# Optimization experiments

Hardware: AMD Instinct MI355X
Metric: run time of the kernel (lower is better)

Reference implementation:

```python
import jax, jax.numpy as jnp
import numpy as np

B, T, F, E, H = 1024, 128, 32, 16, 20
EPS = 1e-3  # keras BatchNormalization default epsilon
D = T * F   # flatten dim; fc1 builds with units = T*F due to pre-build units mutation


def lstm_relu(x, Wk, Wr, b, return_seq):
    """Keras LSTM with activation='relu', recurrent_activation=sigmoid.
    Gate order i, f, c(g), o. x: [B,T,Fin]. Returns [B,T,H] or [B,H]."""
    Bn = x.shape[0]
    h0 = jnp.zeros((Bn, H), x.dtype)
    c0 = jnp.zeros((Bn, H), x.dtype)

    def step(carry, xt):
        h, c = carry
        z = xt @ Wk + h @ Wr + b                      # [B, 4H]
        i, f, g, o = jnp.split(z, 4, axis=-1)
        i = jax.nn.sigmoid(i)
        f = jax.nn.sigmoid(f)
        g = jax.nn.relu(g)
        o = jax.nn.sigmoid(o)
        c = f * c + i * g
        h = o * jax.nn.relu(c)
        return (h, c), h

    (hT, _), hs = jax.lax.scan(step, (h0, c0), jnp.swapaxes(x, 0, 1))
    return jnp.swapaxes(hs, 0, 1) if return_seq else hT


def setup_inputs():
    key = jax.random.key(0)
    ks = jax.random.split(key, 16)
    s = 0.1
    d = {}
    d["x"] = jax.random.normal(ks[0], (B, T, F), jnp.float32)
    # BatchNorm (inference: moving stats)
    d["bn_gamma"] = jnp.ones((F,), jnp.float32)
    d["bn_beta"] = jnp.zeros((F,), jnp.float32)
    d["bn_mean"] = jax.random.normal(ks[1], (F,), jnp.float32) * 0.1
    d["bn_var"] = jax.random.uniform(ks[2], (F,), jnp.float32, 0.5, 1.5)
    # Per-expert LSTM stacks (stacked over expert axis E)
    d["k1"] = jax.random.normal(ks[3], (E, F, 4 * H), jnp.float32) * s
    d["r1"] = jax.random.normal(ks[4], (E, H, 4 * H), jnp.float32) * s
    d["b1"] = jnp.zeros((E, 4 * H), jnp.float32)
    d["k2"] = jax.random.normal(ks[5], (E, H, 4 * H), jnp.float32) * s
    d["r2"] = jax.random.normal(ks[6], (E, H, 4 * H), jnp.float32) * s
    d["b2"] = jnp.zeros((E, 4 * H), jnp.float32)
    d["dw"] = jax.random.normal(ks[7], (E, H, 1), jnp.float32) * s
    d["db"] = jnp.zeros((E, 1), jnp.float32)
    # Gating path: flatten -> Dense(D, relu) -> Dense(E, softmax)
    d["fc1_w"] = jax.random.normal(ks[8], (D, D), jnp.float32) * 0.02
    d["fc1_b"] = jnp.zeros((D,), jnp.float32)
    d["gate_w"] = jax.random.normal(ks[9], (D, E), jnp.float32) * 0.02
    d["gate_b"] = jnp.zeros((E,), jnp.float32)
    return d


def reference(x, bn_gamma, bn_beta, bn_mean, bn_var,
              k1, r1, b1, k2, r2, b2, dw, db,
              fc1_w, fc1_b, gate_w, gate_b):
    # BatchNorm (inference) over last axis
    xn = (x - bn_mean) * jax.lax.rsqrt(bn_var + EPS) * bn_gamma + bn_beta

    def run_expert(k1e, r1e, b1e, k2e, r2e, b2e, dwe, dbe):
        h1 = lstm_relu(xn, k1e, r1e, b1e, return_seq=True)    # [B,T,H]
        h2 = lstm_relu(h1, k2e, r2e, b2e, return_seq=False)   # [B,H]
        return h2 @ dwe + dbe                                  # [B,1]

    expert_outputs = jax.vmap(run_expert)(k1, r1, b1, k2, r2, b2, dw, db)  # [E,B,1]

    flat = x.reshape(x.shape[0], -1)                    # [B, T*F] (raw inputs, not normed)
    g = jax.nn.relu(flat @ fc1_w + fc1_b)               # [B, D]
    w = jax.nn.softmax(g @ gate_w + gate_b, axis=-1)    # [B, E]

    # stack(axis=1) -> [B,E,1]; weights expand_dims(axis=2) -> [B,E,1]; sum over E
    out = jnp.sum(jnp.transpose(expert_outputs, (1, 0, 2)) * w[:, :, None], axis=1)  # [B,1]
    return out
```

## Files before the change

### kernel.cpp

```cpp
#include <hip/hip_runtime.h>
#include <math.h>

#define Bsz 1024
#define Tt  128
#define Ff  32
#define Ee  16
#define Hh  20
#define Dd  4096
#define EPSc 1e-3f
#define LOG2E 1.4426950408889634f

#define PWE 7520

typedef __attribute__((ext_vector_type(8))) short bf16x8;
typedef __attribute__((ext_vector_type(4))) float f32x4;
typedef __attribute__((ext_vector_type(4))) unsigned int u32x4;

#define MFMA16(a,b,c) __builtin_amdgcn_mfma_f32_16x16x32_bf16(a, b, c, 0, 0, 0)

__device__ __forceinline__ float sig2(float z) {
    return __builtin_amdgcn_rcpf(1.0f + __builtin_amdgcn_exp2f(-z));
}
__device__ __forceinline__ unsigned short bf16_rne(float f) {
    unsigned u = __float_as_uint(f);
    u += 0x7FFFu + ((u >> 16) & 1u);
    return (unsigned short)(u >> 16);
}
__device__ __forceinline__ float bf16_to_f(unsigned short h) {
    return __uint_as_float(((unsigned)h) << 16);
}
__device__ __forceinline__ void cvt2(float f0, float f1, unsigned& hp, unsigned& lp) {
    asm("v_cvt_pk_bf16_f32 %0, %1, %2" : "=v"(hp) : "v"(f0), "v"(f1));
    float h0 = __uint_as_float(hp << 16);
    float h1 = __uint_as_float(hp & 0xFFFF0000u);
    asm("v_cvt_pk_bf16_f32 %0, %1, %2" : "=v"(lp) : "v"(f0 - h0), "v"(f1 - h1));
}

__global__ void prep_kernel(const float* __restrict__ x,
                            const float* __restrict__ gamma, const float* __restrict__ beta,
                            const float* __restrict__ mean,  const float* __restrict__ var,
                            unsigned short* __restrict__ xph, unsigned short* __restrict__ xpl,
                            const float* __restrict__ k1, const float* __restrict__ r1,
                            const float* __restrict__ b1, const float* __restrict__ k2,
                            const float* __restrict__ r2, const float* __restrict__ b2,
                            float* __restrict__ pw)
{
    int tid = threadIdx.x;
    if (blockIdx.x < 2048) {
        __shared__ float sc[Ff], sh[Ff];
        if (tid < Ff) {
            float s = gamma[tid] * rsqrtf(var[tid] + EPSc);
            sc[tid] = s;
            sh[tid] = beta[tid] - mean[tid] * s;
        }
        __syncthreads();
        int idx = blockIdx.x * 256 + tid;
        int c   = idx >> 13;
        int rem = idx & 8191;
        int t   = rem >> 6;
        int l   = rem & 63;
        int q   = l >> 4, s = l & 15;
        const float* xr = x + ((size_t)(c * 16 + s) * Tt + t) * Ff + q * 8;
        float4 v0 = *(const float4*)xr;
        float4 v1 = *(const float4*)(xr + 4);
        float xv[8] = {v0.x, v0.y, v0.z, v0.w, v1.x, v1.y, v1.z, v1.w};
        bf16x8 hv, lv;
#pragma unroll
        for (int j = 0; j < 8; ++j) {
            int f = q * 8 + j;
            float xn_ = xv[j] * sc[f] + sh[f];
            unsigned short hi = bf16_rne(xn_);
            hv[j] = (short)hi;
            lv[j] = (short)bf16_rne(xn_ - bf16_to_f(hi));
        }
        *(bf16x8*)(xph + (size_t)idx * 8) = hv;
        *(bf16x8*)(xpl + (size_t)idx * 8) = lv;
    } else {
        int idx = (blockIdx.x - 2048) * 256 + tid;
        if (idx >= Ee * PWE) return;
        int e = idx / PWE;
        int o = idx % PWE;
        float v;
        int g;
        if (o < 7360) {
            int c = o % 80, u = c >> 2;
            g = c & 3;
            int co = g * 20 + u;
            if (o < 2560) {
                int kk = o / 80;
                v = k1[((size_t)e * Ff + kk) * 80 + co];
            } else if (o < 4160) {
                int kk = (o - 2560) / 80;
                v = r1[((size_t)e * Hh + kk) * 80 + co];
            } else if (o < 5760) {
                int kk = (o - 4160) / 80;
                v = k2[((size_t)e * Hh + kk) * 80 + co];
            } else {
                int kk = (o - 5760) / 80;
                v = r2[((size_t)e * Hh + kk) * 80 + co];
            }
        } else if (o < 7440) {
            int c = o - 7360, u = c >> 2;
            g = c & 3;
            v = b1[(size_t)e * 80 + g * 20 + u];
        } else {
            int c = o - 7440, u = c >> 2;
            g = c & 3;
            v = b2[(size_t)e * 80 + g * 20 + u];
        }
        if (g != 2) v *= LOG2E;
        pw[idx] = v;
    }
}

__global__ __launch_bounds__(256, 2) void fused_kernel(
    const unsigned short* __restrict__ xph, const unsigned short* __restrict__ xpl,
    const float* __restrict__ pw, const float* __restrict__ dw, const float* __restrict__ db,
    float* __restrict__ eo,
    const float* __restrict__ x, const float* __restrict__ W,
    const float* __restrict__ bias, float* __restrict__ C)
{
    __shared__ __align__(16) char smem[65536];

    if (blockIdx.x < 256) {
        const int l = threadIdx.x & 63;
        const int q = l >> 4, s = l & 15;
        const int tile = (blockIdx.x << 2) + (threadIdx.x >> 6);
        const int e = tile >> 6;
        const int c = tile & 63;
        const int b0 = c * 16;

        const float* Wm = pw + (size_t)e * PWE;
        bf16x8 K1h[5], K1l[5], R1h[5], R1l[5], K2h[5], K2l[5], R2h[5], R2l[5];
#pragma unroll
        for (int n = 0; n < 5; ++n) {
#pragma unroll
            for (int j = 0; j < 8; ++j) {
                int k8 = q * 8 + j;
                int uk = 4 * j + q;
                int cc = n * 16 + s;
                float wv_;
                unsigned short hi; float hf;
                wv_ = Wm[k8 * 80 + cc];
                hi = bf16_rne(wv_); hf = bf16_to_f(hi);
                K1h[n][j] = (short)hi; K1l[n][j] = (short)bf16_rne(wv_ - hf);
                wv_ = (j < 5) ? Wm[2560 + uk * 80 + cc] : 0.f;
                hi = bf16_rne(wv_); hf = bf16_to_f(hi);
                R1h[n][j] = (short)hi; R1l[n][j] = (short)bf16_rne(wv_ - hf);
                wv_ = (j < 5) ? Wm[4160 + uk * 80 + cc] : 0.f;
                hi = bf16_rne(wv_); hf = bf16_to_f(hi);
                K2h[n][j] = (short)hi; K2l[n][j] = (short)bf16_rne(wv_ - hf);
                wv_ = (j < 5) ? Wm[5760 + uk * 80 + cc] : 0.f;
                hi = bf16_rne(wv_); hf = bf16_to_f(hi);
                R2h[n][j] = (short)hi; R2l[n][j] = (short)bf16_rne(wv_ - hf);
            }
        }
        f32x4 bf1[5], bf2[5];
        float dwr[5];
#pragma unroll
        for (int n = 0; n < 5; ++n) {
            bf1[n] = *(const f32x4*)&Wm[7360 + n * 16 + 4 * q];
            bf2[n] = *(const f32x4*)&Wm[7440 + n * 16 + 4 * q];
            dwr[n] = dw[e * Hh + 4 * n + q];
        }

        float c1[5] = {0, 0, 0, 0, 0}, c2[5] = {0, 0, 0, 0, 0};
        float h2reg[5] = {0, 0, 0, 0, 0};

        const bf16x8 z8 = {0, 0, 0, 0, 0, 0, 0, 0};
        bf16x8 H1a = z8, H1b = z8, H2a = z8, H2b = z8;

        const unsigned short* xbh = xph + (size_t)c * 65536 + l * 8;
        const unsigned short* xbl = xpl + (size_t)c * 65536 + l * 8;
        bf16x8 xch = *(const bf16x8*)xbh;
        bf16x8 xcl = *(const bf16x8*)xbl;

#pragma unroll 1
        for (int t = 0; t < Tt; ++t) {
            bf16x8 xnh = xch, xnl = xcl;
            if (t < Tt - 1) {
                xnh = *(const bf16x8*)(xbh + (t + 1) * 512);
                xnl = *(const bf16x8*)(xbl + (t + 1) * 512);
            }

            f32x4 a1[5];
#pragma unroll
            for (int n = 0; n < 5; ++n) {
                f32x4 acc = bf1[n];
                acc = MFMA16(K1h[n], xch, acc);
                acc = MFMA16(K1l[n], xch, acc);
                acc = MFMA16(K1h[n], xcl, acc);
                acc = MFMA16(R1h[n], H1a, acc);
                acc = MFMA16(R1l[n], H1a, acc);
                acc = MFMA16(R1h[n], H1b, acc);
                a1[n] = acc;
            }
            {
                float hv[5];
#pragma unroll
                for (int n = 0; n < 5; ++n) {
                    float iv = sig2(a1[n][0]);
                    float fv = sig2(a1[n][1]);
                    float gv = fmaxf(a1[n][2], 0.f);
                    float ov = sig2(a1[n][3]);
                    c1[n] = fv * c1[n] + iv * gv;
                    hv[n] = ov * fmaxf(c1[n], 0.f);
                }
                unsigned h0, h1, h2, l0, l1, l2;
                cvt2(hv[0], hv[1], h0, l0);
                cvt2(hv[2], hv[3], h1, l1);
                cvt2(hv[4], 0.f,   h2, l2);
                u32x4 uh = {h0, h1, h2, 0u}, ul = {l0, l1, l2, 0u};
                H1a = __builtin_bit_cast(bf16x8, uh);
                H1b = __builtin_bit_cast(bf16x8, ul);
            }

            f32x4 a2[5];
#pragma unroll
            for (int n = 0; n < 5; ++n) {
                f32x4 acc = bf2[n];
                acc = MFMA16(R2h[n], H2a, acc);
                acc = MFMA16(R2l[n], H2a, acc);
                acc = MFMA16(R2h[n], H2b, acc);
                acc = MFMA16(K2h[n], H1a, acc);
                acc = MFMA16(K2l[n], H1a, acc);
                acc = MFMA16(K2h[n], H1b, acc);
                a2[n] = acc;
            }
            {
                float hv[5];
#pragma unroll
                for (int n = 0; n < 5; ++n) {
                    float iv = sig2(a2[n][0]);
                    float fv = sig2(a2[n][1]);
                    float gv = fmaxf(a2[n][2], 0.f);
                    float ov = sig2(a2[n][3]);
                    c2[n] = fv * c2[n] + iv * gv;
                    float h = ov * fmaxf(c2[n], 0.f);
                    h2reg[n] = h;
                    hv[n] = h;
                }
                unsigned h0, h1, h2, l0, l1, l2;
                cvt2(hv[0], hv[1], h0, l0);
                cvt2(hv[2], hv[3], h1, l1);
                cvt2(hv[4], 0.f,   h2, l2);
                u32x4 uh = {h0, h1, h2, 0u}, ul = {l0, l1, l2, 0u};
                H2a = __builtin_bit_cast(bf16x8, uh);
                H2b = __builtin_bit_cast(bf16x8, ul);
            }

            xch = xnh; xcl = xnl;
        }

        float p = 0.f;
#pragma unroll
        for (int n = 0; n < 5; ++n) p += h2reg[n] * dwr[n];
        p += __shfl_xor(p, 16);
        p += __shfl_xor(p, 32);
        if (q == 0) eo[(size_t)e * Bsz + b0 + s] = db[e] + p;

    } else {
        const int tid = threadIdx.x;
        const int wv = tid >> 6, l = tid & 63, q = l >> 4, s = l & 15;
        const int id = blockIdx.x & 255;
        const int n0 = (id & 31) * 128, m0 = (id >> 5) * 128;
        const int wr = (wv & 1) * 64, wc = (wv >> 1) * 64;

        const int wn = tid & 127, wkq = tid >> 7;
        const int r7w = wn & 7;
        const int pw0 = ((2 * wkq)     ^ r7w) * 8;
        const int pw1 = ((2 * wkq + 1) ^ r7w) * 8;
        const int pw2 = ((4 + 2 * wkq) ^ r7w) * 8;
        const int pw3 = ((5 + 2 * wkq) ^ r7w) * 8;
        const float* WG = W + (size_t)(wkq * 16) * Dd + n0 + wn;

        const int ar = tid >> 3, ac = tid & 7;
        const int akc = ac >> 1, ahalf = ac & 1;
        const int pa_h = ((akc       ^ (ar & 7)) << 3) + ahalf * 4;
        const int pa_l = (((4 + akc) ^ (ar & 7)) << 3) + ahalf * 4;
        const float* AG = x + (size_t)(m0 + ar) * Dd + 4 * ac;

        const int r7r = s & 7;
        const int pfh = (q ^ r7r) * 8;
        const int pfl = ((4 + q) ^ r7r) * 8;

        unsigned short* lds = (unsigned short*)smem;
        unsigned short* c0 = lds;
        unsigned short* c1 = lds + 16384;

        f32x4 acc[4][4];
#pragma unroll
        for (int mt = 0; mt < 4; ++mt)
#pragma unroll
            for (int nt = 0; nt < 4; ++nt) acc[mt][nt] = (f32x4){0.f, 0.f, 0.f, 0.f};

        float wA[16], wB[16];
        float4 aA[4], aB[4];

#define KBARRIER()                                                         \
        {                                                                  \
            asm volatile("s_waitcnt lgkmcnt(0)" ::: "memory");             \
            __builtin_amdgcn_s_barrier();                                  \
            asm volatile("" ::: "memory");                                 \
        }

#define LOADW(dst, kk)                                                     \
        {                                                                  \
            const int kw_ = (kk);                                          \
            _Pragma("unroll")                                              \
            for (int i_ = 0; i_ < 16; ++i_)                                \
                dst[i_] = WG[(size_t)(kw_ + i_) * Dd];                     \
        }
#define LOADA(dst, kk)                                                     \
        {                                                                  \
            const int ka_ = (kk);                                          \
            _Pragma("unroll")                                              \
            for (int p_ = 0; p_ < 4; ++p_)                                 \
                dst[p_] = *(const float4*)(AG + (size_t)(32 * p_) * Dd + ka_); \
        }
#define STAGEW(dst, src)                                                   \
        {                                                                  \
            uint4 h0, l0, h1, l1;                                          \
            cvt2(src[0],  src[1],  h0.x, l0.x); cvt2(src[2],  src[3],  h0.y, l0.y); \
            cvt2(src[4],  src[5],  h0.z, l0.z); cvt2(src[6],  src[7],  h0.w, l0.w); \
            cvt2(src[8],  src[9],  h1.x, l1.x); cvt2(src[10], src[11], h1.y, l1.y); \
            cvt2(src[12], src[13], h1.z, l1.z); cvt2(src[14], src[15], h1.w, l1.w); \
            unsigned short* rb_ = (dst) + wn * 64;                         \
            *(uint4*)&rb_[pw0] = h0;                                       \
            *(uint4*)&rb_[pw1] = h1;                                       \
            *(uint4*)&rb_[pw2] = l0;                                       \
            *(uint4*)&rb_[pw3] = l1;                                       \
        }
#define STAGEA(dst, src)                                                   \
        {                                                                  \
            _Pragma("unroll")                                              \
            for (int p_ = 0; p_ < 4; ++p_) {                               \
                unsigned h0_, l0_, h1_, l1_;                               \
                cvt2(src[p_].x, src[p_].y, h0_, l0_);                      \
                cvt2(src[p_].z, src[p_].w, h1_, l1_);                      \
                unsigned short* rb_ = (dst) + 8192 + (ar + 32 * p_) * 64;  \
                uint2 hv_ = {h0_, h1_}, lv_ = {l0_, l1_};                  \
                *(uint2*)&rb_[pa_h] = hv_;                                 \
                *(uint2*)&rb_[pa_l] = lv_;                                 \
            }                                                              \
        }
#define COMPUTE(cb)                                                        \
        {                                                                  \
            bf16x8 Wfh[4], Wfl[4], Afh[4], Afl[4];                         \
            _Pragma("unroll")                                              \
            for (int nt = 0; nt < 4; ++nt) {                               \
                const unsigned short* rb_ = (cb) + (wc + nt * 16 + s) * 64; \
                Wfh[nt] = *(bf16x8*)&rb_[pfh];                             \
                Wfl[nt] = *(bf16x8*)&rb_[pfl];                             \
            }                                                              \
            _Pragma("unroll")                                              \
            for (int mt = 0; mt < 4; ++mt) {                               \
                const unsigned short* ra_ = (cb) + 8192 + (wr + mt * 16 + s) * 64; \
                Afh[mt] = *(bf16x8*)&ra_[pfh];                             \
                Afl[mt] = *(bf16x8*)&ra_[pfl];                             \
            }                                                              \
            _Pragma("unroll")                                              \
            for (int mt = 0; mt < 4; ++mt)                                 \
                _Pragma("unroll")                                          \
                for (int nt = 0; nt < 4; ++nt) {                           \
                    f32x4 a_ = acc[mt][nt];                                \
                    a_ = MFMA16(Afl[mt], Wfh[nt], a_);                     \
                    a_ = MFMA16(Afh[mt], Wfl[nt], a_);                     \
                    a_ = MFMA16(Afh[mt], Wfh[nt], a_);                     \
                    acc[mt][nt] = a_;                                      \
                }                                                          \
        }

        {
            float w0[16]; float4 a0[4];
            LOADW(w0, 0); LOADA(a0, 0);
            STAGEW(c0, w0); STAGEA(c0, a0);
            LOADW(wA, 32); LOADA(aA, 32);
            LOADW(wB, 64); LOADA(aB, 64);
            __syncthreads();
        }

#pragma unroll 1
        for (int it = 0; it < 128; it += 2) {
            STAGEW(c1, wA); STAGEA(c1, aA);
            {
                const int kk = (it + 3 < 128) ? (it + 3) * 32 : 0;
                LOADW(wA, kk); LOADA(aA, kk);
            }
            COMPUTE(c0);
            KBARRIER();

            if (it + 2 < 128) { STAGEW(c0, wB); STAGEA(c0, aB); }
            {
                const int kk = (it + 4 < 128) ? (it + 4) * 32 : 0;
                LOADW(wB, kk); LOADA(aB, kk);
            }
            COMPUTE(c1);
            KBARRIER();
        }
#undef KBARRIER
#undef LOADW
#undef LOADA
#undef STAGEW
#undef STAGEA
#undef COMPUTE

#pragma unroll
        for (int nt = 0; nt < 4; ++nt) {
            float bv = bias[n0 + wc + nt * 16 + s];
#pragma unroll
            for (int mt = 0; mt < 4; ++mt)
#pragma unroll
                for (int r = 0; r < 4; ++r) {
                    int m = m0 + wr + mt * 16 + q * 4 + r;
                    C[(size_t)m * Dd + n0 + wc + nt * 16 + s] = fmaxf(acc[mt][nt][r] + bv, 0.f);
                }
        }
    }
}

__global__ __launch_bounds__(256) void gate_kernel(const float* __restrict__ g,
                                                   const float* __restrict__ gw,
                                                   const float* __restrict__ gb,
                                                   const float* __restrict__ eo,
                                                   float* __restrict__ out)
{
    int b0 = blockIdx.x * 4;
    int tid = threadIdx.x;
    int lane = tid & 63;
    int wv = tid >> 6;

    float acc[4][16];
#pragma unroll
    for (int bb = 0; bb < 4; ++bb)
#pragma unroll
        for (int j = 0; j < 16; ++j) acc[bb][j] = 0.f;

    const float* g0 = g + (size_t)b0 * Dd;
#pragma unroll
    for (int it = 0; it < Dd / 256; ++it) {
        int d = tid + it * 256;
        const float4* wr_ = (const float4*)(gw + (size_t)d * 16);
        float4 w0 = wr_[0], w1 = wr_[1], w2 = wr_[2], w3 = wr_[3];
        float gv[4];
#pragma unroll
        for (int bb = 0; bb < 4; ++bb) gv[bb] = g0[(size_t)bb * Dd + d];
#pragma unroll
        for (int bb = 0; bb < 4; ++bb) {
            float v = gv[bb];
            acc[bb][0]  += v * w0.x;  acc[bb][1]  += v * w0.y;
            acc[bb][2]  += v * w0.z;  acc[bb][3]  += v * w0.w;
            acc[bb][4]  += v * w1.x;  acc[bb][5]  += v * w1.y;
            acc[bb][6]  += v * w1.z;  acc[bb][7]  += v * w1.w;
            acc[bb][8]  += v * w2.x;  acc[bb][9]  += v * w2.y;
            acc[bb][10] += v * w2.z;  acc[bb][11] += v * w2.w;
            acc[bb][12] += v * w3.x;  acc[bb][13] += v * w3.y;
            acc[bb][14] += v * w3.z;  acc[bb][15] += v * w3.w;
        }
    }

    __shared__ float red[4][4][16];
    __shared__ float logits[4][16];
#pragma unroll
    for (int bb = 0; bb < 4; ++bb)
#pragma unroll
        for (int j = 0; j < 16; ++j) {
            float v = acc[bb][j];
#pragma unroll
            for (int m = 32; m >= 1; m >>= 1) v += __shfl_xor(v, m);
            if (lane == 0) red[wv][bb][j] = v;
        }
    __syncthreads();
    if (tid < 64) {
        int bb = tid >> 4, j = tid & 15;
        logits[bb][j] = gb[j] + red[0][bb][j] + red[1][bb][j] + red[2][bb][j] + red[3][bb][j];
    }
    __syncthreads();
    if (tid < 4) {
        int b = b0 + tid;
        float m = logits[tid][0];
#pragma unroll
        for (int j = 1; j < 16; ++j) m = fmaxf(m, logits[tid][j]);
        float ex[16], ssum = 0.f;
#pragma unroll
        for (int j = 0; j < 16; ++j) { ex[j] = __expf(logits[tid][j] - m); ssum += ex[j]; }
        float inv = 1.f / ssum;
        float o = 0.f;
#pragma unroll
        for (int j = 0; j < 16; ++j) o += ex[j] * inv * eo[(size_t)j * Bsz + b];
        out[b] = o;
    }
}

extern "C" void kernel_launch(void* const* d_in, const int* in_sizes, int n_in,
                              void* d_out, int out_size, void* d_ws, size_t ws_size,
                              hipStream_t stream)
{
    const float* x     = (const float*)d_in[0];
    const float* gamma = (const float*)d_in[1];
    const float* beta  = (const float*)d_in[2];
    const float* mean  = (const float*)d_in[3];
    const float* var   = (const float*)d_in[4];
    const float* k1    = (const float*)d_in[5];
    const float* r1    = (const float*)d_in[6];
    const float* b1    = (const float*)d_in[7];
    const float* k2    = (const float*)d_in[8];
    const float* r2    = (const float*)d_in[9];
    const float* b2    = (const float*)d_in[10];
    const float* dw    = (const float*)d_in[11];
    const float* db    = (const float*)d_in[12];
    const float* fc1w  = (const float*)d_in[13];
    const float* fc1b  = (const float*)d_in[14];
    const float* gw    = (const float*)d_in[15];
    const float* gb    = (const float*)d_in[16];
    float* out = (float*)d_out;

    float* g = (float*)d_ws;
    unsigned short* xph = (unsigned short*)(g + (size_t)Bsz * Dd);
    unsigned short* xpl = xph + (size_t)Bsz * Dd / 2 * 2;
    float* pw  = (float*)(xpl + (size_t)4194304);
    float* eo  = pw + (size_t)Ee * PWE;

    prep_kernel<<<2048 + (Ee * PWE + 255) / 256, 256, 0, stream>>>(
        x, gamma, beta, mean, var, xph, xpl, k1, r1, b1, k2, r2, b2, pw);
    fused_kernel<<<512, 256, 0, stream>>>(xph, xpl, pw, dw, db, eo, x, fc1w, fc1b, g);
    gate_kernel<<<Bsz / 4, 256, 0, stream>>>(g, gw, gb, eo, out);
}
```

Measured before the change: 401.6 us.

## Split-K the fc1 GEMM in two with atomic accumulation and single LDS buffer

The fc1 GEMM blocks are split into two K halves (512 GEMM blocks instead of 256), each accumulating into a zeroed output via atomicAdd. ReLU is deferred to the gate kernel, and the prep kernel now zeroes the output buffer. LDS is halved to a single buffer with extra barriers so three blocks fit per CU, raising occupancy alongside the LSTM blocks. The costs are atomic traffic, an extra zeroing pass, and less overlap between LDS staging and compute.

```diff
diff --git a/kernel.cpp b/kernel.cpp
--- a/kernel.cpp
+++ b/kernel.cpp
@@ -43,7 +43,7 @@
                             const float* __restrict__ k1, const float* __restrict__ r1,
                             const float* __restrict__ b1, const float* __restrict__ k2,
                             const float* __restrict__ r2, const float* __restrict__ b2,
-                            float* __restrict__ pw)
+                            float* __restrict__ pw, float* __restrict__ gz)
 {
     int tid = threadIdx.x;
     if (blockIdx.x < 2048) {
@@ -75,7 +75,7 @@
         }
         *(bf16x8*)(xph + (size_t)idx * 8) = hv;
         *(bf16x8*)(xpl + (size_t)idx * 8) = lv;
-    } else {
+    } else if (blockIdx.x < 2518) {
         int idx = (blockIdx.x - 2048) * 256 + tid;
         if (idx >= Ee * PWE) return;
         int e = idx / PWE;
@@ -110,17 +110,20 @@
         }
         if (g != 2) v *= LOG2E;
         pw[idx] = v;
+    } else {
+        int idx = (blockIdx.x - 2518) * 256 + tid;
+        *(float4*)(gz + (size_t)idx * 4) = (float4){0.f, 0.f, 0.f, 0.f};
     }
 }
 
-__global__ __launch_bounds__(256, 2) void fused_kernel(
+__global__ __launch_bounds__(256, 3) void fused_kernel(
     const unsigned short* __restrict__ xph, const unsigned short* __restrict__ xpl,
     const float* __restrict__ pw, const float* __restrict__ dw, const float* __restrict__ db,
     float* __restrict__ eo,
     const float* __restrict__ x, const float* __restrict__ W,
     const float* __restrict__ bias, float* __restrict__ C)
 {
-    __shared__ __align__(16) char smem[65536];
+    __shared__ __align__(16) char smem[32768];
 
     if (blockIdx.x < 256) {
         const int l = threadIdx.x & 63;
@@ -262,7 +265,10 @@
     } else {
         const int tid = threadIdx.x;
         const int wv = tid >> 6, l = tid & 63, q = l >> 4, s = l & 15;
-        const int id = blockIdx.x & 255;
+        const int fb = blockIdx.x - 256;
+        const int id = fb & 255;
+        const int kh = fb >> 8;
+        const int kbase = kh * 2048;
         const int n0 = (id & 31) * 128, m0 = (id >> 5) * 128;
         const int wr = (wv & 1) * 64, wc = (wv >> 1) * 64;
 
@@ -272,21 +278,19 @@
         const int pw1 = ((2 * wkq + 1) ^ r7w) * 8;
         const int pw2 = ((4 + 2 * wkq) ^ r7w) * 8;
         const int pw3 = ((5 + 2 * wkq) ^ r7w) * 8;
-        const float* WG = W + (size_t)(wkq * 16) * Dd + n0 + wn;
+        const float* WG = W + (size_t)(kbase + wkq * 16) * Dd + n0 + wn;
 
         const int ar = tid >> 3, ac = tid & 7;
         const int akc = ac >> 1, ahalf = ac & 1;
         const int pa_h = ((akc       ^ (ar & 7)) << 3) + ahalf * 4;
         const int pa_l = (((4 + akc) ^ (ar & 7)) << 3) + ahalf * 4;
-        const float* AG = x + (size_t)(m0 + ar) * Dd + 4 * ac;
+        const float* AG = x + (size_t)(m0 + ar) * Dd + 4 * ac + kbase;
 
         const int r7r = s & 7;
         const int pfh = (q ^ r7r) * 8;
         const int pfl = ((4 + q) ^ r7r) * 8;
 
         unsigned short* lds = (unsigned short*)smem;
-        unsigned short* c0 = lds;
-        unsigned short* c1 = lds + 16384;
 
         f32x4 acc[4][4];
 #pragma unroll
@@ -374,29 +378,29 @@
         {
             float w0[16]; float4 a0[4];
             LOADW(w0, 0); LOADA(a0, 0);
-            STAGEW(c0, w0); STAGEA(c0, a0);
+            STAGEW(lds, w0); STAGEA(lds, a0);
             LOADW(wA, 32); LOADA(aA, 32);
             LOADW(wB, 64); LOADA(aB, 64);
-            __syncthreads();
         }
 
 #pragma unroll 1
-        for (int it = 0; it < 128; it += 2) {
-            STAGEW(c1, wA); STAGEA(c1, aA);
+        for (int it = 0; it < 64; it += 2) {
+            KBARRIER();
+            COMPUTE(lds);
+            KBARRIER();
+            STAGEW(lds, wA); STAGEA(lds, aA);
             {
-                const int kk = (it + 3 < 128) ? (it + 3) * 32 : 0;
+                const int kk = (it + 3 < 64) ? (it + 3) * 32 : 0;
                 LOADW(wA, kk); LOADA(aA, kk);
             }
-            COMPUTE(c0);
             KBARRIER();
-
-            if (it + 2 < 128) { STAGEW(c0, wB); STAGEA(c0, aB); }
+            COMPUTE(lds);
+            KBARRIER();
+            if (it + 2 < 64) { STAGEW(lds, wB); STAGEA(lds, aB); }
             {
-                const int kk = (it + 4 < 128) ? (it + 4) * 32 : 0;
+                const int kk = (it + 4 < 64) ? (it + 4) * 32 : 0;
                 LOADW(wB, kk); LOADA(aB, kk);
             }
-            COMPUTE(c1);
-            KBARRIER();
         }
 #undef KBARRIER
 #undef LOADW
@@ -407,13 +411,14 @@
 
 #pragma unroll
         for (int nt = 0; nt < 4; ++nt) {
-            float bv = bias[n0 + wc + nt * 16 + s];
+            float bv = (kh == 0) ? bias[n0 + wc + nt * 16 + s] : 0.f;
 #pragma unroll
             for (int mt = 0; mt < 4; ++mt)
 #pragma unroll
                 for (int r = 0; r < 4; ++r) {
                     int m = m0 + wr + mt * 16 + q * 4 + r;
-                    C[(size_t)m * Dd + n0 + wc + nt * 16 + s] = fmaxf(acc[mt][nt][r] + bv, 0.f);
+                    atomicAdd(&C[(size_t)m * Dd + n0 + wc + nt * 16 + s],
+                              acc[mt][nt][r] + bv);
                 }
         }
     }
@@ -444,7 +449,7 @@
         float4 w0 = wr_[0], w1 = wr_[1], w2 = wr_[2], w3 = wr_[3];
         float gv[4];
 #pragma unroll
-        for (int bb = 0; bb < 4; ++bb) gv[bb] = g0[(size_t)bb * Dd + d];
+        for (int bb = 0; bb < 4; ++bb) gv[bb] = fmaxf(g0[(size_t)bb * Dd + d], 0.f);
 #pragma unroll
         for (int bb = 0; bb < 4; ++bb) {
             float v = gv[bb];
@@ -521,8 +526,8 @@
     float* pw  = (float*)(xpl + (size_t)4194304);
     float* eo  = pw + (size_t)Ee * PWE;
 
-    prep_kernel<<<2048 + (Ee * PWE + 255) / 256, 256, 0, stream>>>(
-        x, gamma, beta, mean, var, xph, xpl, k1, r1, b1, k2, r2, b2, pw);
-    fused_kernel<<<512, 256, 0, stream>>>(xph, xpl, pw, dw, db, eo, x, fc1w, fc1b, g);
+    prep_kernel<<<2518 + 4096, 256, 0, stream>>>(
+        x, gamma, beta, mean, var, xph, xpl, k1, r1, b1, k2, r2, b2, pw, g);
+    fused_kernel<<<768, 256, 0, stream>>>(xph, xpl, pw, dw, db, eo, x, fc1w, fc1b, g);
     gate_kernel<<<Bsz / 4, 256, 0, stream>>>(g, gw, gb, eo, out);
 }
```

Result: slower. 1.151 ms (+186.6%).
